# Optimization experiments

Hardware: AMD Instinct MI355X
Metric: run time of the kernel (lower is better)

## Reference

```python
import jax, jax.numpy as jnp
import numpy as np
from math import sqrt

B, L, H, E = 8, 2048, 16, 128
S = 256  # selected_freq_count


def setup_inputs() -> dict:
    key = jax.random.key(0)
    kq, kk, kv = jax.random.split(key, 3)
    rng = np.random.default_rng(0)
    # unique sorted indices in [0, L//2), mirroring get_random_frequencies
    index_q = jnp.asarray(np.sort(rng.choice(L // 2, size=S, replace=False)), dtype=jnp.int32)
    index_kv = jnp.asarray(np.sort(rng.choice(L // 2, size=S, replace=False)), dtype=jnp.int32)
    return {
        "q": jax.random.normal(kq, (B, L, H, E), dtype=jnp.float32),
        "k": jax.random.normal(kk, (B, L, H, E), dtype=jnp.float32),
        "v": jax.random.normal(kv, (B, L, H, E), dtype=jnp.float32),
        "attn_mask": jnp.zeros((1,), dtype=jnp.int32),  # unused by the module
        "index_q": index_q,
        "index_kv": index_kv,
    }


def reference(q, k, v, attn_mask, index_q, index_kv):
    b, l, h, e = q.shape
    scale = 1.0 / sqrt(e)
    # permute to [B, H, E, L] then gather selected frequency columns
    xq = jnp.transpose(q, (0, 2, 3, 1))  # bhel
    xk = jnp.transpose(k, (0, 2, 3, 1))  # bhel
    xq_ft = jnp.take(xq, index_q, axis=-1)   # [B,H,E,Sq]
    xk_ft = jnp.take(xk, index_kv, axis=-1)  # [B,H,E,Sk]
    # dense attention on the gathered subset (contract over E)
    xqk = jax.nn.softmax(scale * jnp.einsum('bhex,bhey->bhxy', xq_ft, xk_ft), axis=-1)
    # NOTE: original multiplies attention by xk_ft_ (v is unused) -- faithful
    xqkv = jnp.einsum('bhxy,bhey->bhex', xqk, xk_ft)  # [B,H,E,Sq]
    # scatter back into zero-initialized [B,H,E,L]
    out_ft = jnp.zeros((b, h, e, l), dtype=q.dtype).at[..., index_q].set(xqkv)
    return out_ft, xqk
```

## Files before the change

kernel.cpp:

```cpp
#include <hip/hip_runtime.h>
#include <math.h>

#define NB 8
#define NL 2048
#define NH 16
#define NE 128
#define NS 256
#define XT 64
#define NXB (NS/XT)

__global__ __launch_bounds__(256) void fsa_main(
    const float* __restrict__ q, const float* __restrict__ k,
    const int* __restrict__ iq, const int* __restrict__ ikv,
    float* __restrict__ out_ft, float* __restrict__ out_p)
{
  __shared__ __align__(16) char smem[87040];
  float* Qs  = (float*)smem;
  float* Ks1 = (float*)(smem + 32768);
  float* Pl  = (float*)smem;
  float* Ks2 = (float*)(smem + 69632);

  const int t  = threadIdx.x;
  const int bh = blockIdx.x / NXB;
  const int xb = blockIdx.x % NXB;
  const int b  = bh / NH;
  const int h  = bh % NH;
  const int x0 = xb * XT;

  const int tx = t >> 5;
  const int ty = t & 31;

  {
    const int e4  = t & 31;
    const int xr0 = t >> 5;
    #pragma unroll
    for (int p = 0; p < 8; ++p) {
      const int xr = xr0 + 8*p;
      const int lq = iq[x0 + xr];
      const float4 vv = *(const float4*)(q + (size_t)((b*NL + lq)*NH + h)*NE + 4*e4);
      *(float4*)(Qs + xr*NE + 4*e4) = vv;
    }
  }

  float acc[8][8];
  #pragma unroll
  for (int i = 0; i < 8; ++i)
    #pragma unroll
    for (int j = 0; j < 8; ++j) acc[i][j] = 0.f;

  for (int ec = 0; ec < 8; ++ec) {
    __syncthreads();
    {
      const int e4 = t & 3;
      const int yb = t >> 2;
      #pragma unroll
      for (int p = 0; p < 4; ++p) {
        const int y  = yb + 64*p;
        const int lk = ikv[y];
        const float4 vv = *(const float4*)(k + (size_t)((b*NL + lk)*NH + h)*NE + ec*16 + 4*e4);
        Ks1[(4*e4+0)*257 + y] = vv.x;
        Ks1[(4*e4+1)*257 + y] = vv.y;
        Ks1[(4*e4+2)*257 + y] = vv.z;
        Ks1[(4*e4+3)*257 + y] = vv.w;
      }
    }
    __syncthreads();
    #pragma unroll
    for (int eq = 0; eq < 4; ++eq) {
      float kv[4][8];
      #pragma unroll
      for (int e = 0; e < 4; ++e)
        #pragma unroll
        for (int j = 0; j < 8; ++j)
          kv[e][j] = Ks1[(eq*4 + e)*257 + ty + 32*j];
      #pragma unroll
      for (int i = 0; i < 8; ++i) {
        const float4 q4 = *(const float4*)(Qs + (tx*8 + i)*NE + ec*16 + eq*4);
        #pragma unroll
        for (int j = 0; j < 8; ++j) {
          acc[i][j] = fmaf(q4.x, kv[0][j], acc[i][j]);
          acc[i][j] = fmaf(q4.y, kv[1][j], acc[i][j]);
          acc[i][j] = fmaf(q4.z, kv[2][j], acc[i][j]);
          acc[i][j] = fmaf(q4.w, kv[3][j], acc[i][j]);
        }
      }
    }
  }

  const float scale = 0.08838834764831845f;
  #pragma unroll
  for (int i = 0; i < 8; ++i) {
    float m = -3.4e38f;
    #pragma unroll
    for (int j = 0; j < 8; ++j) { acc[i][j] *= scale; m = fmaxf(m, acc[i][j]); }
    #pragma unroll
    for (int o = 16; o >= 1; o >>= 1) m = fmaxf(m, __shfl_xor(m, o));
    float s = 0.f;
    #pragma unroll
    for (int j = 0; j < 8; ++j) { acc[i][j] = __expf(acc[i][j] - m); s += acc[i][j]; }
    #pragma unroll
    for (int o = 16; o >= 1; o >>= 1) s += __shfl_xor(s, o);
    const float inv = 1.0f / s;
    #pragma unroll
    for (int j = 0; j < 8; ++j) acc[i][j] *= inv;
  }

  __syncthreads();

  {
    float* outp = out_p + ((size_t)bh*NS + x0)*NS;
    #pragma unroll
    for (int i = 0; i < 8; ++i) {
      const int x = tx*8 + i;
      #pragma unroll
      for (int j = 0; j < 8; ++j) {
        const int y = ty + 32*j;
        Pl[y*68 + x]    = acc[i][j];
        outp[x*NS + y]  = acc[i][j];
      }
    }
  }

  float acc2[2][16];
  #pragma unroll
  for (int n = 0; n < 2; ++n)
    #pragma unroll
    for (int m = 0; m < 16; ++m) acc2[n][m] = 0.f;

  const int c = t & 31;
  const int r = t >> 5;

  for (int yc = 0; yc < 8; ++yc) {
    __syncthreads();
    {
      const int e4 = t & 7;
      const int yy = t >> 3;
      const int lk = ikv[yc*32 + yy];
      const float* src = k + (size_t)((b*NL + lk)*NH + h)*NE;
      #pragma unroll
      for (int p = 0; p < 4; ++p) {
        const float4 vv = *(const float4*)(src + 4*e4 + 32*p);
        *(float4*)(Ks2 + yy*132 + 4*e4 + 32*p) = vv;
      }
    }
    __syncthreads();
    for (int yy = 0; yy < 32; ++yy) {
      const float p0 = Pl[(yc*32 + yy)*68 + c];
      const float p1 = Pl[(yc*32 + yy)*68 + c + 32];
      float4 kv4[4];
      #pragma unroll
      for (int qd = 0; qd < 4; ++qd)
        kv4[qd] = *(const float4*)(Ks2 + yy*132 + r*16 + 4*qd);
      const float* kvf = (const float*)kv4;
      #pragma unroll
      for (int m = 0; m < 16; ++m) {
        acc2[0][m] = fmaf(p0, kvf[m], acc2[0][m]);
        acc2[1][m] = fmaf(p1, kvf[m], acc2[1][m]);
      }
    }
  }

  {
    float* outf = out_ft + (size_t)bh*NE*NL;
    #pragma unroll
    for (int n = 0; n < 2; ++n) {
      const int x  = x0 + c + 32*n;
      const int lq = iq[x];
      #pragma unroll
      for (int m = 0; m < 16; ++m) {
        const int e = r*16 + m;
        outf[(size_t)e*NL + lq] = acc2[n][m];
      }
    }
  }
}

extern "C" void kernel_launch(void* const* d_in, const int* in_sizes, int n_in,
                              void* d_out, int out_size, void* d_ws, size_t ws_size,
                              hipStream_t stream) {
  const float* q   = (const float*)d_in[0];
  const float* k   = (const float*)d_in[1];
  const int* iq    = (const int*)d_in[4];
  const int* ikv   = (const int*)d_in[5];
  float* out       = (float*)d_out;

  const size_t out_ft_elems = (size_t)NB*NH*NE*NL;
  hipMemsetAsync(out, 0, out_ft_elems * sizeof(float), stream);

  fsa_main<<<dim3(NB*NH*NXB), dim3(256), 0, stream>>>(
      q, k, iq, ikv, out, out + out_ft_elems);
}
```

Before: 442.1 us.

## Rewrite attention with bf16 MFMA and replace memset-scatter with compact write plus expand

Both GEMMs (QK^T and P·K) now use bf16 MFMA 16x16x32 instructions instead of scalar fp32 FMAs. Q and K are converted to bf16 when staged into shared memory, with padded strides. The memset plus scattered output write is replaced by a compact write followed by a second kernel that builds each full row through an inverse index table, so every output row is written in one coalesced pass. The grid order is swizzled and occupancy hints are added. The bf16 inputs and probabilities lose precision compared with the fp32 reference.

```diff
diff --git a/kernel.cpp b/kernel.cpp
--- a/kernel.cpp
+++ b/kernel.cpp
@@ -1,5 +1,9 @@
 #include <hip/hip_runtime.h>
 #include <math.h>
+
+typedef __bf16 bf16_t;
+typedef __attribute__((ext_vector_type(8))) __bf16 bf16x8;
+typedef __attribute__((ext_vector_type(4))) float f32x4;
 
 #define NB 8
 #define NL 2048
@@ -7,170 +11,203 @@
 #define NE 128
 #define NS 256
 #define XT 64
-#define NXB (NS/XT)
-
-__global__ __launch_bounds__(256) void fsa_main(
+
+#define QSTR 136
+#define PSTR 72
+
+__global__ __launch_bounds__(256, 3) void fsa_gemm(
     const float* __restrict__ q, const float* __restrict__ k,
     const int* __restrict__ iq, const int* __restrict__ ikv,
-    float* __restrict__ out_ft, float* __restrict__ out_p)
+    float* __restrict__ out)
 {
-  __shared__ __align__(16) char smem[87040];
-  float* Qs  = (float*)smem;
-  float* Ks1 = (float*)(smem + 32768);
-  float* Pl  = (float*)smem;
-  float* Ks2 = (float*)(smem + 69632);
-
-  const int t  = threadIdx.x;
-  const int bh = blockIdx.x / NXB;
-  const int xb = blockIdx.x % NXB;
-  const int b  = bh / NH;
-  const int h  = bh % NH;
+  float* out_ft = out;
+  float* out_p  = out + (size_t)NB*NH*NE*NL;
+
+  __shared__ __align__(16) char smem[34816];
+  bf16_t* Qs = (bf16_t*)smem;
+  bf16_t* Ks = (bf16_t*)(smem + 17408);
+  bf16_t* Ps = (bf16_t*)smem;
+  bf16_t* Kt = (bf16_t*)(smem + 9216);
+
+  const int t = threadIdx.x;
+  const int tile = (blockIdx.x & 7) * 64 + (blockIdx.x >> 3);
+  const int bh = tile >> 2, xb = tile & 3;
+  const int b = bh >> 4, h = bh & 15;
   const int x0 = xb * XT;
 
-  const int tx = t >> 5;
-  const int ty = t & 31;
-
-  {
-    const int e4  = t & 31;
-    const int xr0 = t >> 5;
+  const int w   = t >> 6;
+  const int l15 = t & 15;
+  const int lg  = (t & 63) >> 4;
+
+  {
+    const int e4 = t & 31, xr = t >> 5;
     #pragma unroll
     for (int p = 0; p < 8; ++p) {
-      const int xr = xr0 + 8*p;
-      const int lq = iq[x0 + xr];
-      const float4 vv = *(const float4*)(q + (size_t)((b*NL + lq)*NH + h)*NE + 4*e4);
-      *(float4*)(Qs + xr*NE + 4*e4) = vv;
-    }
-  }
-
-  float acc[8][8];
-  #pragma unroll
-  for (int i = 0; i < 8; ++i)
-    #pragma unroll
-    for (int j = 0; j < 8; ++j) acc[i][j] = 0.f;
-
-  for (int ec = 0; ec < 8; ++ec) {
+      const int x  = xr + 8*p;
+      const int lq = iq[x0 + x];
+      const float4 v = *(const float4*)(q + ((size_t)(b*NL + lq)*NH + h)*NE + 4*e4);
+      union { bf16_t h4[4]; uint2 u; } pk;
+      pk.h4[0]=(bf16_t)v.x; pk.h4[1]=(bf16_t)v.y; pk.h4[2]=(bf16_t)v.z; pk.h4[3]=(bf16_t)v.w;
+      *(uint2*)(Qs + x*QSTR + 4*e4) = pk.u;
+    }
+  }
+
+  f32x4 acc1[16];
+  #pragma unroll
+  for (int i = 0; i < 16; ++i) acc1[i] = (f32x4){0.f,0.f,0.f,0.f};
+  bf16x8 aQ[4];
+
+  #pragma unroll
+  for (int c = 0; c < 4; ++c) {
+    if (c > 0) __syncthreads();
+    {
+      const int e4 = t & 31, yr = t >> 5;
+      #pragma unroll
+      for (int p = 0; p < 8; ++p) {
+        const int y  = yr + 8*p;
+        const int lk = ikv[c*64 + y];
+        const float4 v = *(const float4*)(k + ((size_t)(b*NL + lk)*NH + h)*NE + 4*e4);
+        union { bf16_t h4[4]; uint2 u; } pk;
+        pk.h4[0]=(bf16_t)v.x; pk.h4[1]=(bf16_t)v.y; pk.h4[2]=(bf16_t)v.z; pk.h4[3]=(bf16_t)v.w;
+        *(uint2*)(Ks + y*QSTR + 4*e4) = pk.u;
+      }
+    }
+    __syncthreads();
+    if (c == 0) {
+      #pragma unroll
+      for (int ks = 0; ks < 4; ++ks)
+        aQ[ks] = *(const bf16x8*)(Qs + (w*16 + l15)*QSTR + ks*32 + lg*8);
+    }
+    #pragma unroll
+    for (int ks = 0; ks < 4; ++ks) {
+      #pragma unroll
+      for (int yt = 0; yt < 4; ++yt) {
+        const bf16x8 bk = *(const bf16x8*)(Ks + (yt*16 + l15)*QSTR + ks*32 + lg*8);
+        acc1[c*4 + yt] = __builtin_amdgcn_mfma_f32_16x16x32_bf16(aQ[ks], bk, acc1[c*4 + yt], 0, 0, 0);
+      }
+    }
+  }
+
+  const float scale = 0.08838834764831845f;
+  #pragma unroll
+  for (int r = 0; r < 4; ++r) {
+    float m = -3.4e38f;
+    #pragma unroll
+    for (int yt = 0; yt < 16; ++yt) { acc1[yt][r] *= scale; m = fmaxf(m, acc1[yt][r]); }
+    m = fmaxf(m, __shfl_xor(m, 1)); m = fmaxf(m, __shfl_xor(m, 2));
+    m = fmaxf(m, __shfl_xor(m, 4)); m = fmaxf(m, __shfl_xor(m, 8));
+    float s = 0.f;
+    #pragma unroll
+    for (int yt = 0; yt < 16; ++yt) { const float e = __expf(acc1[yt][r] - m); acc1[yt][r] = e; s += e; }
+    s += __shfl_xor(s, 1); s += __shfl_xor(s, 2); s += __shfl_xor(s, 4); s += __shfl_xor(s, 8);
+    const float inv = 1.0f / s;
+    #pragma unroll
+    for (int yt = 0; yt < 16; ++yt) acc1[yt][r] *= inv;
+  }
+
+  {
+    float* po = out_p + ((size_t)bh*NS + x0 + w*16 + lg*4)*NS + l15;
+    #pragma unroll
+    for (int r = 0; r < 4; ++r)
+      #pragma unroll
+      for (int yt = 0; yt < 16; ++yt)
+        po[(size_t)r*NS + yt*16] = acc1[yt][r];
+  }
+
+  f32x4 acc2[2][4];
+  #pragma unroll
+  for (int et = 0; et < 2; ++et)
+    #pragma unroll
+    for (int xt = 0; xt < 4; ++xt) acc2[et][xt] = (f32x4){0.f,0.f,0.f,0.f};
+
+  #pragma unroll
+  for (int c = 0; c < 4; ++c) {
     __syncthreads();
     {
-      const int e4 = t & 3;
-      const int yb = t >> 2;
+      const int xr = w*16 + lg*4;
+      #pragma unroll
+      for (int r = 0; r < 4; ++r)
+        #pragma unroll
+        for (int yt = 0; yt < 4; ++yt)
+          Ps[(xr + r)*PSTR + yt*16 + l15] = (bf16_t)acc1[c*4 + yt][r];
+    }
+    {
+      const int e4 = t & 31, yb = t >> 5;
       #pragma unroll
       for (int p = 0; p < 4; ++p) {
-        const int y  = yb + 64*p;
-        const int lk = ikv[y];
-        const float4 vv = *(const float4*)(k + (size_t)((b*NL + lk)*NH + h)*NE + ec*16 + 4*e4);
-        Ks1[(4*e4+0)*257 + y] = vv.x;
-        Ks1[(4*e4+1)*257 + y] = vv.y;
-        Ks1[(4*e4+2)*257 + y] = vv.z;
-        Ks1[(4*e4+3)*257 + y] = vv.w;
+        const int y0  = 2*(yb + 8*p);
+        const int lk0 = ikv[c*64 + y0];
+        const int lk1 = ikv[c*64 + y0 + 1];
+        const float4 va = *(const float4*)(k + ((size_t)(b*NL + lk0)*NH + h)*NE + 4*e4);
+        const float4 vb = *(const float4*)(k + ((size_t)(b*NL + lk1)*NH + h)*NE + 4*e4);
+        union { bf16_t h2[2]; unsigned u; } pr;
+        pr.h2[0]=(bf16_t)va.x; pr.h2[1]=(bf16_t)vb.x; *(unsigned*)(Kt + (4*e4+0)*PSTR + y0) = pr.u;
+        pr.h2[0]=(bf16_t)va.y; pr.h2[1]=(bf16_t)vb.y; *(unsigned*)(Kt + (4*e4+1)*PSTR + y0) = pr.u;
+        pr.h2[0]=(bf16_t)va.z; pr.h2[1]=(bf16_t)vb.z; *(unsigned*)(Kt + (4*e4+2)*PSTR + y0) = pr.u;
+        pr.h2[0]=(bf16_t)va.w; pr.h2[1]=(bf16_t)vb.w; *(unsigned*)(Kt + (4*e4+3)*PSTR + y0) = pr.u;
       }
     }
     __syncthreads();
     #pragma unroll
-    for (int eq = 0; eq < 4; ++eq) {
-      float kv[4][8];
-      #pragma unroll
-      for (int e = 0; e < 4; ++e)
-        #pragma unroll
-        for (int j = 0; j < 8; ++j)
-          kv[e][j] = Ks1[(eq*4 + e)*257 + ty + 32*j];
-      #pragma unroll
-      for (int i = 0; i < 8; ++i) {
-        const float4 q4 = *(const float4*)(Qs + (tx*8 + i)*NE + ec*16 + eq*4);
-        #pragma unroll
-        for (int j = 0; j < 8; ++j) {
-          acc[i][j] = fmaf(q4.x, kv[0][j], acc[i][j]);
-          acc[i][j] = fmaf(q4.y, kv[1][j], acc[i][j]);
-          acc[i][j] = fmaf(q4.z, kv[2][j], acc[i][j]);
-          acc[i][j] = fmaf(q4.w, kv[3][j], acc[i][j]);
-        }
-      }
-    }
-  }
-
-  const float scale = 0.08838834764831845f;
-  #pragma unroll
-  for (int i = 0; i < 8; ++i) {
-    float m = -3.4e38f;
-    #pragma unroll
-    for (int j = 0; j < 8; ++j) { acc[i][j] *= scale; m = fmaxf(m, acc[i][j]); }
-    #pragma unroll
-    for (int o = 16; o >= 1; o >>= 1) m = fmaxf(m, __shfl_xor(m, o));
-    float s = 0.f;
-    #pragma unroll
-    for (int j = 0; j < 8; ++j) { acc[i][j] = __expf(acc[i][j] - m); s += acc[i][j]; }
-    #pragma unroll
-    for (int o = 16; o >= 1; o >>= 1) s += __shfl_xor(s, o);
-    const float inv = 1.0f / s;
-    #pragma unroll
-    for (int j = 0; j < 8; ++j) acc[i][j] *= inv;
-  }
-
+    for (int ks = 0; ks < 2; ++ks) {
+      const bf16x8 aK0 = *(const bf16x8*)(Kt + (w*32 +  0 + l15)*PSTR + ks*32 + lg*8);
+      const bf16x8 aK1 = *(const bf16x8*)(Kt + (w*32 + 16 + l15)*PSTR + ks*32 + lg*8);
+      #pragma unroll
+      for (int xt = 0; xt < 4; ++xt) {
+        const bf16x8 bp = *(const bf16x8*)(Ps + (xt*16 + l15)*PSTR + ks*32 + lg*8);
+        acc2[0][xt] = __builtin_amdgcn_mfma_f32_16x16x32_bf16(aK0, bp, acc2[0][xt], 0, 0, 0);
+        acc2[1][xt] = __builtin_amdgcn_mfma_f32_16x16x32_bf16(aK1, bp, acc2[1][xt], 0, 0, 0);
+      }
+    }
+  }
+
+  #pragma unroll
+  for (int et = 0; et < 2; ++et)
+    #pragma unroll
+    for (int xt = 0; xt < 4; ++xt)
+      #pragma unroll
+      for (int r = 0; r < 4; ++r) {
+        const int e = w*32 + et*16 + lg*4 + r;
+        out_ft[((size_t)bh*NE + e)*NL + x0 + xt*16 + l15] = acc2[et][xt][r];
+      }
+}
+
+__global__ __launch_bounds__(256) void fsa_expand(
+    const int* __restrict__ iq, float* __restrict__ out_ft)
+{
+  __shared__ int   inv[NL];
+  __shared__ float oc[8][NS];
+  const int t  = threadIdx.x;
+  const int bh = blockIdx.x >> 4;
+  const int eg = blockIdx.x & 15;
+
+  {
+    const int4 mi = {-1,-1,-1,-1};
+    *(int4*)(inv + 8*t)     = mi;
+    *(int4*)(inv + 8*t + 4) = mi;
+  }
   __syncthreads();
-
-  {
-    float* outp = out_p + ((size_t)bh*NS + x0)*NS;
-    #pragma unroll
-    for (int i = 0; i < 8; ++i) {
-      const int x = tx*8 + i;
-      #pragma unroll
-      for (int j = 0; j < 8; ++j) {
-        const int y = ty + 32*j;
-        Pl[y*68 + x]    = acc[i][j];
-        outp[x*NS + y]  = acc[i][j];
-      }
-    }
-  }
-
-  float acc2[2][16];
-  #pragma unroll
-  for (int n = 0; n < 2; ++n)
-    #pragma unroll
-    for (int m = 0; m < 16; ++m) acc2[n][m] = 0.f;
-
-  const int c = t & 31;
-  const int r = t >> 5;
-
-  for (int yc = 0; yc < 8; ++yc) {
-    __syncthreads();
-    {
-      const int e4 = t & 7;
-      const int yy = t >> 3;
-      const int lk = ikv[yc*32 + yy];
-      const float* src = k + (size_t)((b*NL + lk)*NH + h)*NE;
-      #pragma unroll
-      for (int p = 0; p < 4; ++p) {
-        const float4 vv = *(const float4*)(src + 4*e4 + 32*p);
-        *(float4*)(Ks2 + yy*132 + 4*e4 + 32*p) = vv;
-      }
-    }
-    __syncthreads();
-    for (int yy = 0; yy < 32; ++yy) {
-      const float p0 = Pl[(yc*32 + yy)*68 + c];
-      const float p1 = Pl[(yc*32 + yy)*68 + c + 32];
-      float4 kv4[4];
-      #pragma unroll
-      for (int qd = 0; qd < 4; ++qd)
-        kv4[qd] = *(const float4*)(Ks2 + yy*132 + r*16 + 4*qd);
-      const float* kvf = (const float*)kv4;
-      #pragma unroll
-      for (int m = 0; m < 16; ++m) {
-        acc2[0][m] = fmaf(p0, kvf[m], acc2[0][m]);
-        acc2[1][m] = fmaf(p1, kvf[m], acc2[1][m]);
-      }
-    }
-  }
-
-  {
-    float* outf = out_ft + (size_t)bh*NE*NL;
-    #pragma unroll
-    for (int n = 0; n < 2; ++n) {
-      const int x  = x0 + c + 32*n;
-      const int lq = iq[x];
-      #pragma unroll
-      for (int m = 0; m < 16; ++m) {
-        const int e = r*16 + m;
-        outf[(size_t)e*NL + lq] = acc2[n][m];
-      }
+  inv[iq[t]] = t;
+  {
+    const int row = t >> 5, c0 = (t & 31) * 8;
+    const float* src = out_ft + ((size_t)bh*NE + eg*8 + row)*NL;
+    *(float4*)&oc[row][c0]     = *(const float4*)(src + c0);
+    *(float4*)&oc[row][c0 + 4] = *(const float4*)(src + c0 + 4);
+  }
+  __syncthreads();
+
+  #pragma unroll
+  for (int r = 0; r < 8; ++r) {
+    float* dst = out_ft + ((size_t)bh*NE + eg*8 + r)*NL;
+    #pragma unroll
+    for (int sg = 0; sg < 2; ++sg) {
+      const int l = 8*t + 4*sg;
+      float4 v;
+      { const int i0 = inv[l+0]; v.x = (i0 >= 0) ? oc[r][i0] : 0.f; }
+      { const int i1 = inv[l+1]; v.y = (i1 >= 0) ? oc[r][i1] : 0.f; }
+      { const int i2 = inv[l+2]; v.z = (i2 >= 0) ? oc[r][i2] : 0.f; }
+      { const int i3 = inv[l+3]; v.w = (i3 >= 0) ? oc[r][i3] : 0.f; }
+      *(float4*)(dst + l) = v;
     }
   }
 }
@@ -178,15 +215,12 @@
 extern "C" void kernel_launch(void* const* d_in, const int* in_sizes, int n_in,
                               void* d_out, int out_size, void* d_ws, size_t ws_size,
                               hipStream_t stream) {
-  const float* q   = (const float*)d_in[0];
-  const float* k   = (const float*)d_in[1];
-  const int* iq    = (const int*)d_in[4];
-  const int* ikv   = (const int*)d_in[5];
-  float* out       = (float*)d_out;
-
-  const size_t out_ft_elems = (size_t)NB*NH*NE*NL;
-  hipMemsetAsync(out, 0, out_ft_elems * sizeof(float), stream);
-
-  fsa_main<<<dim3(NB*NH*NXB), dim3(256), 0, stream>>>(
-      q, k, iq, ikv, out, out + out_ft_elems);
+  const float* q = (const float*)d_in[0];
+  const float* k = (const float*)d_in[1];
+  const int* iq  = (const int*)d_in[4];
+  const int* ikv = (const int*)d_in[5];
+  float* out = (float*)d_out;
+
+  fsa_gemm<<<dim3(NB*NH*(NS/XT)), dim3(256), 0, stream>>>(q, k, iq, ikv, out);
+  fsa_expand<<<dim3(NB*NH*16), dim3(256), 0, stream>>>(iq, out);
 }
```

Result: faster. 366.7 us (-17.1%).
